# Optimization experiments

Measured on AMD Instinct MI355X. Metric: run time of the kernel, lower is better.

Reference implementation:

```python
import jax, jax.numpy as jnp
import numpy as np

ALPHA = 0.8  # LeakyReLU negative slope (nn.LeakyReLU(self.alpha))
OUT_DIM = 64
EDGE_DIM = 32


def setup_inputs() -> dict:
    key = jax.random.key(0)
    ks = jax.random.split(key, 6)
    N, S, IN_D = 50000, 16, 128
    xav = lambda k, shp: jax.random.uniform(k, shp, jnp.float32, -1.0, 1.0) * (1.414 * np.sqrt(6.0 / (shp[0] + shp[1])))
    return {
        "input": jax.random.normal(ks[0], (N, IN_D), jnp.float32),
        "neigh_feat": jax.random.normal(ks[1], (N * S, IN_D), jnp.float32),
        "edge_emb": jax.random.normal(ks[2], (N * S, EDGE_DIM), jnp.float32),
        "W": xav(ks[3], (IN_D, OUT_DIM)),
        "W2": xav(ks[4], (IN_D, OUT_DIM)),
        "a": xav(ks[5], (2 * OUT_DIM + EDGE_DIM, 1)),
    }


def reference(input, neigh_feat, edge_emb, W, W2, a):
    N = input.shape[0]
    S = neigh_feat.shape[0] // N
    D = W.shape[1]
    E = edge_emb.shape[1]

    x = input @ W                               # [N, D]
    neighs = (neigh_feat @ W2).reshape(N, S, D)  # [N, S, D]
    ee = edge_emb.reshape(N, S, E)               # [N, S, E]

    # a_input = cat([x_rep, neighs, ee], -1); e = leakyrelu(a_input @ a)
    # Split a to avoid materializing the concatenated [N, S, 2D+E] tensor.
    a_x, a_n, a_e = a[:D, 0], a[D:2 * D, 0], a[2 * D:, 0]
    scores = (x @ a_x)[:, None] + neighs @ a_n + ee @ a_e   # [N, S]
    e = jnp.where(scores > 0, scores, ALPHA * scores)        # LeakyReLU

    attention = jax.nn.softmax(e, axis=1)        # softmax over neighbors
    # dropout is a no-op in eval mode (training=False)

    h_prime = jnp.einsum("ns,nsd->nd", attention, neighs)    # [N, D]
    h_edge = jnp.einsum("ns,nse->ne", attention, ee)         # [N, E]

    # concat_node=True, concat_edge=True, activation=None
    return jnp.concatenate([x, h_prime, h_edge], axis=1)      # [N, 2D+E]
```

## Files before the change

### kernel.cpp

```cpp
#include <hip/hip_runtime.h>


#define NGS 136
#define EES 40

#define BAR() do {                                              \
    asm volatile("s_waitcnt lgkmcnt(0)" ::: "memory");          \
    __builtin_amdgcn_s_barrier();                               \
    asm volatile("" ::: "memory");                              \
} while (0)

__global__ __launch_bounds__(256)
void prep_kernel(const float* __restrict__ W2,
                 const float* __restrict__ a,
                 float* __restrict__ ws) {
    const int t = threadIdx.x;
    __shared__ float s_a[160];
    if (t < 160) { float v = a[t]; s_a[t] = v; ws[128 + t] = v; }
    __syncthreads();
    if (t < 128) {
        float p = 0.f;
        #pragma unroll
        for (int d = 0; d < 64; d++) p = fmaf(W2[t * 64 + d], s_a[64 + d], p);
        ws[t] = p;
    }
}

__global__ __launch_bounds__(256)
void gat_kernel(const float* __restrict__ input,
                const float* __restrict__ neigh,
                const float* __restrict__ edge,
                const float* __restrict__ W,
                const float* __restrict__ W2,
                const float* __restrict__ ws,
                float* __restrict__ out,
                int N) {
    const int t = threadIdx.x;
    const int d = t & 63;
    const int q = t >> 6;

    __shared__ float s_ws[288];
    __shared__ float s_in[128];
    __shared__ float s_ng[16 * NGS];
    __shared__ float s_ee[16 * EES];
    __shared__ float s_redA[256];
    __shared__ float s_redE[256];
    __shared__ float s_agg[128];
    __shared__ float s_sc[16];
    __shared__ float s_att[16];

    float rW[32], rW2[32];
    {
        const int kb = q * 32;
        #pragma unroll
        for (int k = 0; k < 32; k++) {
            rW[k]  = W [(kb + k) * 64 + d];
            rW2[k] = W2[(kb + k) * 64 + d];
        }
    }
    s_ws[t] = ws[t];
    if (t < 32) s_ws[256 + t] = ws[256 + t];

    const int stride = gridDim.x;
    int n = blockIdx.x;

    {
        const float4* ng4 = (const float4*)(neigh + (size_t)n * 2048);
        const float4 a0 = ng4[t];
        const float4 a1 = ng4[t + 256];
        float4 b0;
        if (t < 128)      b0 = ((const float4*)(edge  + (size_t)n * 512))[t];
        else if (t < 160) b0 = ((const float4*)(input + (size_t)n * 128))[t - 128];
        {
            float* dst = s_ng + (t >> 5) * NGS + ((t & 31) << 2);
            dst[0] = a0.x; dst[1] = a0.y; dst[2] = a0.z; dst[3] = a0.w;
            const int i2 = t + 256;
            float* dst2 = s_ng + (i2 >> 5) * NGS + ((i2 & 31) << 2);
            dst2[0] = a1.x; dst2[1] = a1.y; dst2[2] = a1.z; dst2[3] = a1.w;
        }
        if (t < 128) {
            float* dst = s_ee + (t >> 3) * EES + ((t & 7) << 2);
            dst[0] = b0.x; dst[1] = b0.y; dst[2] = b0.z; dst[3] = b0.w;
        } else if (t < 160) {
            float* dst = s_in + ((t - 128) << 2);
            dst[0] = b0.x; dst[1] = b0.y; dst[2] = b0.z; dst[3] = b0.w;
        }
    }
    BAR();

    for (; n < N; n += stride) {
        const int nn = n + stride;
        const bool pf = nn < N;
        float4 p_a0, p_a1, p_b0;
        if (pf) {
            const float4* ng4 = (const float4*)(neigh + (size_t)nn * 2048);
            p_a0 = ng4[t];
            p_a1 = ng4[t + 256];
            if (t < 128)      p_b0 = ((const float4*)(edge  + (size_t)nn * 512))[t];
            else if (t < 160) p_b0 = ((const float4*)(input + (size_t)nn * 128))[t - 128];
        }

        {
            const int kb = q * 32;
            float p = 0.f;
            #pragma unroll
            for (int k = 0; k < 32; k++) p = fmaf(s_in[kb + k], rW[k], p);
            s_redA[t] = p;
        }
        {
            const int s = t >> 4, g = t & 15;
            float p = 0.f;
            #pragma unroll
            for (int j = 0; j < 8; j++) {
                const int k = g + (j << 4);
                p = fmaf(s_ng[s * NGS + k], s_ws[k], p);
            }
            #pragma unroll
            for (int j = 0; j < 2; j++) {
                const int e = g + (j << 4);
                p = fmaf(s_ee[s * EES + e], s_ws[256 + e], p);
            }
            #pragma unroll
            for (int off = 8; off; off >>= 1) p += __shfl_down(p, off, 16);
            if (g == 0) s_sc[s] = p;
        }
        BAR();

        if (t < 64) {
            const float x = s_redA[t] + s_redA[t + 64] + s_redA[t + 128] + s_redA[t + 192];
            out[(size_t)n * 160 + t] = x;
            float p = x * s_ws[128 + t];
            #pragma unroll
            for (int off = 32; off; off >>= 1) p += __shfl_down(p, off, 64);
            const float sx = __shfl(p, 0, 64);
            if (t < 16) {
                const float sc = sx + s_sc[t];
                const float e = sc > 0.f ? sc : 0.8f * sc;
                float m = e;
                #pragma unroll
                for (int off = 8; off; off >>= 1) m = fmaxf(m, __shfl_xor(m, off, 16));
                const float ex = __expf(e - m);
                float sum = ex;
                #pragma unroll
                for (int off = 8; off; off >>= 1) sum += __shfl_xor(sum, off, 16);
                s_att[t] = ex / sum;
            }
        }
        BAR();

        if (t < 128) {
            float p = 0.f;
            #pragma unroll
            for (int s = 0; s < 16; s++) p = fmaf(s_att[s], s_ng[s * NGS + t], p);
            s_agg[t] = p;
        } else if (t < 160) {
            const int e = t - 128;
            float p = 0.f;
            #pragma unroll
            for (int s = 0; s < 16; s++) p = fmaf(s_att[s], s_ee[s * EES + e], p);
            out[(size_t)n * 160 + 128 + e] = p;
        }
        BAR();

        {
            const int kb = q * 32;
            float p = 0.f;
            #pragma unroll
            for (int k = 0; k < 32; k++) p = fmaf(s_agg[kb + k], rW2[k], p);
            s_redE[t] = p;
        }
        if (pf) {
            float* dst = s_ng + (t >> 5) * NGS + ((t & 31) << 2);
            dst[0] = p_a0.x; dst[1] = p_a0.y; dst[2] = p_a0.z; dst[3] = p_a0.w;
            const int i2 = t + 256;
            float* dst2 = s_ng + (i2 >> 5) * NGS + ((i2 & 31) << 2);
            dst2[0] = p_a1.x; dst2[1] = p_a1.y; dst2[2] = p_a1.z; dst2[3] = p_a1.w;
            if (t < 128) {
                float* de = s_ee + (t >> 3) * EES + ((t & 7) << 2);
                de[0] = p_b0.x; de[1] = p_b0.y; de[2] = p_b0.z; de[3] = p_b0.w;
            } else if (t < 160) {
                float* di = s_in + ((t - 128) << 2);
                di[0] = p_b0.x; di[1] = p_b0.y; di[2] = p_b0.z; di[3] = p_b0.w;
            }
        }
        BAR();

        if (t < 64)
            out[(size_t)n * 160 + 64 + t] =
                s_redE[t] + s_redE[t + 64] + s_redE[t + 128] + s_redE[t + 192];
    }
}

extern "C" void kernel_launch(void* const* d_in, const int* in_sizes, int n_in,
                              void* d_out, int out_size, void* d_ws, size_t ws_size,
                              hipStream_t stream) {
    const float* input = (const float*)d_in[0];
    const float* neigh = (const float*)d_in[1];
    const float* edge  = (const float*)d_in[2];
    const float* W     = (const float*)d_in[3];
    const float* W2    = (const float*)d_in[4];
    const float* a     = (const float*)d_in[5];
    float* ws = (float*)d_ws;
    float* out = (float*)d_out;

    const int N = in_sizes[0] / 128;

    prep_kernel<<<1, 256, 0, stream>>>(W2, a, ws);
    gat_kernel<<<1280, 256, 0, stream>>>(input, neigh, edge, W, W2, ws, out, N);
}
```

Baseline: 656.1 us.

## Double-buffer node tiles in LDS via direct global-to-LDS loads by one wave

Replaces the register-staged prefetch with double-buffered shared-memory tiles that one wavefront fills using global_load_lds, so the next node's neighbor, edge and input data stream directly into LDS while the current node is computed. The attention-weighted aggregation moves into the softmax wave using float4 reads. The final per-node output write is deferred into the next iteration, which removes one barrier per node. It also vectorises the shared-memory dot products, sets a 4-block occupancy bound and shrinks the grid to 1024 blocks. The cost is roughly double the LDS footprint, and all loading is serialised onto a single wave.

Result: slower. 837.3 us (+27.6%).

```diff
diff --git a/kernel.cpp b/kernel.cpp
--- a/kernel.cpp
+++ b/kernel.cpp
@@ -1,14 +1,22 @@
 #include <hip/hip_runtime.h>
 
-
-#define NGS 136
-#define EES 40
 
 #define BAR() do {                                              \
     asm volatile("s_waitcnt lgkmcnt(0)" ::: "memory");          \
     __builtin_amdgcn_s_barrier();                               \
     asm volatile("" ::: "memory");                              \
 } while (0)
+
+#define GLDS16(gp, lp) __builtin_amdgcn_global_load_lds(                     \
+    (const __attribute__((address_space(1))) void*)(gp),                     \
+    (__attribute__((address_space(3))) void*)(lp), 16, 0, 0)
+#define GLDS4(gp, lp)  __builtin_amdgcn_global_load_lds(                     \
+    (const __attribute__((address_space(1))) void*)(gp),                     \
+    (__attribute__((address_space(3))) void*)(lp), 4, 0, 0)
+
+__device__ __forceinline__ float dot4(float4 a, float4 b) {
+    return fmaf(a.x, b.x, fmaf(a.y, b.y, fmaf(a.z, b.z, a.w * b.w)));
+}
 
 __global__ __launch_bounds__(256)
 void prep_kernel(const float* __restrict__ W2,
@@ -26,7 +34,7 @@
     }
 }
 
-__global__ __launch_bounds__(256)
+__global__ __launch_bounds__(256, 4)
 void gat_kernel(const float* __restrict__ input,
                 const float* __restrict__ neigh,
                 const float* __restrict__ edge,
@@ -38,11 +46,12 @@
     const int t = threadIdx.x;
     const int d = t & 63;
     const int q = t >> 6;
+    const int lane = t & 63;
 
     __shared__ float s_ws[288];
-    __shared__ float s_in[128];
-    __shared__ float s_ng[16 * NGS];
-    __shared__ float s_ee[16 * EES];
+    __shared__ float s_in[2][128];
+    __shared__ float s_ng[2][2048];
+    __shared__ float s_ee[2][512];
     __shared__ float s_redA[256];
     __shared__ float s_redE[256];
     __shared__ float s_agg[128];
@@ -63,73 +72,74 @@
 
     const int stride = gridDim.x;
     int n = blockIdx.x;
-
-    {
-        const float4* ng4 = (const float4*)(neigh + (size_t)n * 2048);
-        const float4 a0 = ng4[t];
-        const float4 a1 = ng4[t + 256];
-        float4 b0;
-        if (t < 128)      b0 = ((const float4*)(edge  + (size_t)n * 512))[t];
-        else if (t < 160) b0 = ((const float4*)(input + (size_t)n * 128))[t - 128];
+    int n_prev = -1;
+    int cur = 0;
+
+    if (q == 3) {
+        const float* gn = neigh + (size_t)n * 2048;
+        #pragma unroll
+        for (int i = 0; i < 8; i++) GLDS16(gn + i * 256 + lane * 4, &s_ng[0][i * 256]);
+        const float* ge = edge + (size_t)n * 512;
+        #pragma unroll
+        for (int i = 0; i < 2; i++) GLDS16(ge + i * 256 + lane * 4, &s_ee[0][i * 256]);
+        const float* gi = input + (size_t)n * 128;
+        #pragma unroll
+        for (int i = 0; i < 2; i++) GLDS4(gi + i * 64 + lane, &s_in[0][i * 64]);
+        asm volatile("s_waitcnt vmcnt(0)" ::: "memory");
+    }
+    BAR();
+
+    for (; n < N; n += stride, cur ^= 1) {
+        const int nn = n + stride;
+        if (q == 3 && nn < N) {
+            const float* gn = neigh + (size_t)nn * 2048;
+            #pragma unroll
+            for (int i = 0; i < 8; i++) GLDS16(gn + i * 256 + lane * 4, &s_ng[cur ^ 1][i * 256]);
+            const float* ge = edge + (size_t)nn * 512;
+            #pragma unroll
+            for (int i = 0; i < 2; i++) GLDS16(ge + i * 256 + lane * 4, &s_ee[cur ^ 1][i * 256]);
+            const float* gi = input + (size_t)nn * 128;
+            #pragma unroll
+            for (int i = 0; i < 2; i++) GLDS4(gi + i * 64 + lane, &s_in[cur ^ 1][i * 64]);
+        }
+
         {
-            float* dst = s_ng + (t >> 5) * NGS + ((t & 31) << 2);
-            dst[0] = a0.x; dst[1] = a0.y; dst[2] = a0.z; dst[3] = a0.w;
-            const int i2 = t + 256;
-            float* dst2 = s_ng + (i2 >> 5) * NGS + ((i2 & 31) << 2);
-            dst2[0] = a1.x; dst2[1] = a1.y; dst2[2] = a1.z; dst2[3] = a1.w;
-        }
-        if (t < 128) {
-            float* dst = s_ee + (t >> 3) * EES + ((t & 7) << 2);
-            dst[0] = b0.x; dst[1] = b0.y; dst[2] = b0.z; dst[3] = b0.w;
-        } else if (t < 160) {
-            float* dst = s_in + ((t - 128) << 2);
-            dst[0] = b0.x; dst[1] = b0.y; dst[2] = b0.z; dst[3] = b0.w;
-        }
-    }
-    BAR();
-
-    for (; n < N; n += stride) {
-        const int nn = n + stride;
-        const bool pf = nn < N;
-        float4 p_a0, p_a1, p_b0;
-        if (pf) {
-            const float4* ng4 = (const float4*)(neigh + (size_t)nn * 2048);
-            p_a0 = ng4[t];
-            p_a1 = ng4[t + 256];
-            if (t < 128)      p_b0 = ((const float4*)(edge  + (size_t)nn * 512))[t];
-            else if (t < 160) p_b0 = ((const float4*)(input + (size_t)nn * 128))[t - 128];
-        }
-
-        {
-            const int kb = q * 32;
+            const float4* in4 = (const float4*)s_in[cur];
             float p = 0.f;
             #pragma unroll
-            for (int k = 0; k < 32; k++) p = fmaf(s_in[kb + k], rW[k], p);
+            for (int j = 0; j < 8; j++) {
+                const float4 v = in4[q * 8 + j];
+                p = fmaf(v.x, rW[4 * j + 0], p);
+                p = fmaf(v.y, rW[4 * j + 1], p);
+                p = fmaf(v.z, rW[4 * j + 2], p);
+                p = fmaf(v.w, rW[4 * j + 3], p);
+            }
             s_redA[t] = p;
         }
         {
             const int s = t >> 4, g = t & 15;
-            float p = 0.f;
-            #pragma unroll
-            for (int j = 0; j < 8; j++) {
-                const int k = g + (j << 4);
-                p = fmaf(s_ng[s * NGS + k], s_ws[k], p);
-            }
-            #pragma unroll
-            for (int j = 0; j < 2; j++) {
-                const int e = g + (j << 4);
-                p = fmaf(s_ee[s * EES + e], s_ws[256 + e], p);
+            const float4* ng4 = (const float4*)(s_ng[cur] + s * 128);
+            const float4* wa4 = (const float4*)s_ws;
+            float p = dot4(ng4[g], wa4[g]) + dot4(ng4[g + 16], wa4[g + 16]);
+            if (g < 8) {
+                const float4 e4 = ((const float4*)(s_ee[cur] + s * 32))[g];
+                const float4 a4 = ((const float4*)(s_ws + 256))[g];
+                p += dot4(e4, a4);
             }
             #pragma unroll
             for (int off = 8; off; off >>= 1) p += __shfl_down(p, off, 16);
             if (g == 0) s_sc[s] = p;
         }
+        if (q == 0 && n_prev >= 0) {
+            out[(size_t)n_prev * 160 + 64 + d] =
+                s_redE[d] + s_redE[64 + d] + s_redE[128 + d] + s_redE[192 + d];
+        }
         BAR();
 
-        if (t < 64) {
-            const float x = s_redA[t] + s_redA[t + 64] + s_redA[t + 128] + s_redA[t + 192];
-            out[(size_t)n * 160 + t] = x;
-            float p = x * s_ws[128 + t];
+        if (q == 0) {
+            const float x = s_redA[d] + s_redA[64 + d] + s_redA[128 + d] + s_redA[192 + d];
+            out[(size_t)n * 160 + d] = x;
+            float p = x * s_ws[128 + d];
             #pragma unroll
             for (int off = 32; off; off >>= 1) p += __shfl_down(p, off, 64);
             const float sx = __shfl(p, 0, 64);
@@ -145,49 +155,65 @@
                 for (int off = 8; off; off >>= 1) sum += __shfl_xor(sum, off, 16);
                 s_att[t] = ex / sum;
             }
+            asm volatile("s_waitcnt lgkmcnt(0)" ::: "memory");
+            __builtin_amdgcn_sched_barrier(0);
+            float attv[16];
+            #pragma unroll
+            for (int j = 0; j < 4; j++) {
+                const float4 v = ((const float4*)s_att)[j];
+                attv[4 * j + 0] = v.x; attv[4 * j + 1] = v.y;
+                attv[4 * j + 2] = v.z; attv[4 * j + 3] = v.w;
+            }
+            if (t < 32) {
+                const float4* col = (const float4*)s_ng[cur] + t;
+                float4 acc = make_float4(0.f, 0.f, 0.f, 0.f);
+                #pragma unroll
+                for (int s = 0; s < 16; s++) {
+                    const float4 v = col[s * 32];
+                    acc.x = fmaf(attv[s], v.x, acc.x);
+                    acc.y = fmaf(attv[s], v.y, acc.y);
+                    acc.z = fmaf(attv[s], v.z, acc.z);
+                    acc.w = fmaf(attv[s], v.w, acc.w);
+                }
+                ((float4*)s_agg)[t] = acc;
+            } else if (t < 40) {
+                const int e = t - 32;
+                const float4* col = (const float4*)s_ee[cur] + e;
+                float4 acc = make_float4(0.f, 0.f, 0.f, 0.f);
+                #pragma unroll
+                for (int s = 0; s < 16; s++) {
+                    const float4 v = col[s * 8];
+                    acc.x = fmaf(attv[s], v.x, acc.x);
+                    acc.y = fmaf(attv[s], v.y, acc.y);
+                    acc.z = fmaf(attv[s], v.z, acc.z);
+                    acc.w = fmaf(attv[s], v.w, acc.w);
+                }
+                *(float4*)(out + (size_t)n * 160 + 128 + 4 * e) = acc;
+            }
         }
         BAR();
 
-        if (t < 128) {
+        {
+            const float4* ag4 = (const float4*)s_agg;
             float p = 0.f;
             #pragma unroll
-            for (int s = 0; s < 16; s++) p = fmaf(s_att[s], s_ng[s * NGS + t], p);
-            s_agg[t] = p;
-        } else if (t < 160) {
-            const int e = t - 128;
-            float p = 0.f;
-            #pragma unroll
-            for (int s = 0; s < 16; s++) p = fmaf(s_att[s], s_ee[s * EES + e], p);
-            out[(size_t)n * 160 + 128 + e] = p;
-        }
+            for (int j = 0; j < 8; j++) {
+                const float4 v = ag4[q * 8 + j];
+                p = fmaf(v.x, rW2[4 * j + 0], p);
+                p = fmaf(v.y, rW2[4 * j + 1], p);
+                p = fmaf(v.z, rW2[4 * j + 2], p);
+                p = fmaf(v.w, rW2[4 * j + 3], p);
+            }
+            s_redE[t] = p;
+        }
+        if (q == 3) asm volatile("s_waitcnt vmcnt(0)" ::: "memory");
+        n_prev = n;
         BAR();
-
-        {
-            const int kb = q * 32;
-            float p = 0.f;
-            #pragma unroll
-            for (int k = 0; k < 32; k++) p = fmaf(s_agg[kb + k], rW2[k], p);
-            s_redE[t] = p;
-        }
-        if (pf) {
-            float* dst = s_ng + (t >> 5) * NGS + ((t & 31) << 2);
-            dst[0] = p_a0.x; dst[1] = p_a0.y; dst[2] = p_a0.z; dst[3] = p_a0.w;
-            const int i2 = t + 256;
-            float* dst2 = s_ng + (i2 >> 5) * NGS + ((i2 & 31) << 2);
-            dst2[0] = p_a1.x; dst2[1] = p_a1.y; dst2[2] = p_a1.z; dst2[3] = p_a1.w;
-            if (t < 128) {
-                float* de = s_ee + (t >> 3) * EES + ((t & 7) << 2);
-                de[0] = p_b0.x; de[1] = p_b0.y; de[2] = p_b0.z; de[3] = p_b0.w;
-            } else if (t < 160) {
-                float* di = s_in + ((t - 128) << 2);
-                di[0] = p_b0.x; di[1] = p_b0.y; di[2] = p_b0.z; di[3] = p_b0.w;
-            }
-        }
-        BAR();
-
-        if (t < 64)
-            out[(size_t)n * 160 + 64 + t] =
-                s_redE[t] + s_redE[t + 64] + s_redE[t + 128] + s_redE[t + 192];
+    }
+
+    if (q == 0 && n_prev >= 0) {
+        out[(size_t)n_prev * 160 + 64 + d] =
+            s_redE[d] + s_redE[64 + d] + s_redE[128 + d] + s_redE[192 + d];
     }
 }
 
@@ -206,5 +232,5 @@
     const int N = in_sizes[0] / 128;
 
     prep_kernel<<<1, 256, 0, stream>>>(W2, a, ws);
-    gat_kernel<<<1280, 256, 0, stream>>>(input, neigh, edge, W, W2, ws, out, N);
-}
+    gat_kernel<<<1024, 256, 0, stream>>>(input, neigh, edge, W, W2, ws, out, N);
+}
```
